# Optimization experiments

Hardware: AMD Instinct MI355X
Metric: run time of the kernel (lower is better)

## Reference

```python
import jax, jax.numpy as jnp
import numpy as np

N_NODES = 100000
N_EDGES = 600000
D_IN = 128
D_OUT = 128


def setup_inputs() -> dict:
    key = jax.random.key(0)
    ks = jax.random.split(key, 8)
    stdv = 1.0 / np.sqrt(D_OUT)
    return {
        "x": jax.random.normal(ks[0], (N_NODES, D_IN), dtype=jnp.float32),
        "edge_src": jax.random.randint(ks[1], (N_EDGES,), 0, N_NODES, dtype=jnp.int32),
        "edge_dst": jax.random.randint(ks[2], (N_EDGES,), 0, N_NODES, dtype=jnp.int32),
        "edge_weight": jax.random.uniform(ks[3], (N_EDGES,), dtype=jnp.float32),
        "weight_l": jax.random.uniform(ks[4], (D_IN, D_OUT), minval=-stdv, maxval=stdv, dtype=jnp.float32),
        "bias_l": jax.random.uniform(ks[5], (D_OUT,), minval=-stdv, maxval=stdv, dtype=jnp.float32),
        "weight_r": jax.random.uniform(ks[6], (D_IN, D_OUT), minval=-stdv, maxval=stdv, dtype=jnp.float32),
        "bias_r": jax.random.uniform(ks[7], (D_OUT,), minval=-stdv, maxval=stdv, dtype=jnp.float32),
    }


def reference(x, edge_src, edge_dst, edge_weight, weight_l, bias_l, weight_r, bias_r):
    # h = input @ weight_l  -> [N, D_OUT]
    h = x @ weight_l
    # spmm(adj, h): out[dst] += adj[dst, src] * h[src]
    msgs = h[edge_src] * edge_weight[:, None]          # [E, D_OUT] gather
    agg = jax.ops.segment_sum(msgs, edge_dst, num_segments=N_NODES)
    out = agg + bias_l
    # root_weight branch (size is None)
    out = out + x @ weight_r + bias_r
    return out
```

## Files before the change

kernel.cpp:

```cpp
#include <hip/hip_runtime.h>
#include <hip/hip_bf16.h>

#define D 128
#define SCAN_BLK 256
#define SCAN_VPT 4
#define SCAN_TILE (SCAN_BLK * SCAN_VPT)

typedef __attribute__((ext_vector_type(8))) short short8;
typedef __attribute__((ext_vector_type(4))) float f32x4;

__global__ __launch_bounds__(256) void prep_w(
    const float* __restrict__ Wl, const float* __restrict__ Wr,
    const float* __restrict__ bl, const float* __restrict__ br,
    __hip_bfloat16* __restrict__ WTl, __hip_bfloat16* __restrict__ WTr,
    float* __restrict__ bsum, int* __restrict__ deg, int n_nodes) {
  const int tid = blockIdx.x * 256 + threadIdx.x;
  const int n = (tid >> 7) & 127;
  const int k = tid & 127;
  if (tid < 16384) {
    WTl[n * D + k] = __float2bfloat16(Wl[k * D + n]);
  } else {
    WTr[n * D + k] = __float2bfloat16(Wr[k * D + n]);
  }
  if (tid < 128) bsum[tid] = bl[tid] + br[tid];
  for (int i = tid; i < n_nodes; i += 32768) deg[i] = 0;
}

__global__ __launch_bounds__(256) void gemm_hr(
    const float* __restrict__ x, const __hip_bfloat16* __restrict__ WTl,
    const __hip_bfloat16* __restrict__ WTr, const float* __restrict__ bsum,
    __hip_bfloat16* __restrict__ h, float* __restrict__ out,
    const int* __restrict__ edst, int* __restrict__ deg, int n_edges,
    int n_rowtiles) {
  const int gsz = gridDim.x * 256;
  for (int e = blockIdx.x * 256 + threadIdx.x; e < n_edges; e += gsz)
    atomicAdd(&deg[edst[e]], 1);

  __shared__ __hip_bfloat16 xs[16][136];
  const int t = threadIdx.x;
  const int wave = t >> 6;
  const int lane = t & 63;
  const int m = lane & 15;
  const int q = lane >> 4;

  short8 bfl[2][4], bfr[2][4];
  float bias[2];
#pragma unroll
  for (int c = 0; c < 2; ++c) {
    const int n0 = wave * 32 + c * 16;
    bias[c] = bsum[n0 + m];
#pragma unroll
    for (int ks = 0; ks < 4; ++ks) {
      bfl[c][ks] = *(const short8*)&WTl[(n0 + m) * D + ks * 32 + q * 8];
      bfr[c][ks] = *(const short8*)&WTr[(n0 + m) * D + ks * 32 + q * 8];
    }
  }

  const int srow = t >> 4;
  const int scol = (t & 15) * 8;

  for (int rt = blockIdx.x; rt < n_rowtiles; rt += gridDim.x) {
    const int rowbase = rt * 16;
    {
      const float4* src = (const float4*)&x[(size_t)(rowbase + srow) * D + scol];
      const float4 v0 = src[0], v1 = src[1];
      __hip_bfloat16* dst = &xs[srow][scol];
      dst[0] = __float2bfloat16(v0.x); dst[1] = __float2bfloat16(v0.y);
      dst[2] = __float2bfloat16(v0.z); dst[3] = __float2bfloat16(v0.w);
      dst[4] = __float2bfloat16(v1.x); dst[5] = __float2bfloat16(v1.y);
      dst[6] = __float2bfloat16(v1.z); dst[7] = __float2bfloat16(v1.w);
    }
    __syncthreads();

    f32x4 accL[2], accR[2];
#pragma unroll
    for (int c = 0; c < 2; ++c)
#pragma unroll
      for (int r = 0; r < 4; ++r) { accL[c][r] = 0.f; accR[c][r] = 0.f; }

#pragma unroll
    for (int ks = 0; ks < 4; ++ks) {
      const short8 afrag = *(const short8*)&xs[m][ks * 32 + q * 8];
#pragma unroll
      for (int c = 0; c < 2; ++c) {
        accL[c] = __builtin_amdgcn_mfma_f32_16x16x32_bf16(afrag, bfl[c][ks], accL[c], 0, 0, 0);
        accR[c] = __builtin_amdgcn_mfma_f32_16x16x32_bf16(afrag, bfr[c][ks], accR[c], 0, 0, 0);
      }
    }

#pragma unroll
    for (int c = 0; c < 2; ++c) {
      const int n = wave * 32 + c * 16 + m;
#pragma unroll
      for (int r = 0; r < 4; ++r) {
        const size_t row = (size_t)(rowbase + q * 4 + r);
        h[row * D + n] = __float2bfloat16(accL[c][r]);
        out[row * D + n] = accR[c][r] + bias[c];
      }
    }
    __syncthreads();
  }
}

__global__ __launch_bounds__(SCAN_BLK) void scan1_kernel(
    const int* __restrict__ deg, int* __restrict__ offsets,
    int* __restrict__ partials, int n) {
  __shared__ int sdata[SCAN_BLK];
  const int t = threadIdx.x;
  const int base = blockIdx.x * SCAN_TILE + t * SCAN_VPT;

  int v[SCAN_VPT];
  int s = 0;
#pragma unroll
  for (int j = 0; j < SCAN_VPT; ++j) {
    v[j] = (base + j < n) ? deg[base + j] : 0;
    s += v[j];
  }
  sdata[t] = s;
  __syncthreads();
  for (int off = 1; off < SCAN_BLK; off <<= 1) {
    int xv = (t >= off) ? sdata[t - off] : 0;
    __syncthreads();
    sdata[t] += xv;
    __syncthreads();
  }
  int excl = sdata[t] - s;
  if (t == SCAN_BLK - 1) partials[blockIdx.x] = sdata[t];
  int run = excl;
#pragma unroll
  for (int j = 0; j < SCAN_VPT; ++j) {
    if (base + j < n) offsets[base + j] = run;
    run += v[j];
  }
}

__global__ __launch_bounds__(SCAN_BLK) void scan3_kernel(
    int* __restrict__ offsets, int* __restrict__ pos,
    const int* __restrict__ partials, int n, int n_edges) {
  __shared__ int s_add;
  const int t = threadIdx.x;
  if (t < 64) {
    int v = 0;
    for (int j = t; j < blockIdx.x; j += 64) v += partials[j];
#pragma unroll
    for (int off = 32; off > 0; off >>= 1) v += __shfl_down(v, off);
    if (t == 0) s_add = v;
  }
  __syncthreads();
  const int add = s_add;
  const int base = blockIdx.x * SCAN_TILE + t * SCAN_VPT;
#pragma unroll
  for (int j = 0; j < SCAN_VPT; ++j) {
    const int i = base + j;
    if (i < n) {
      const int o = offsets[i] + add;
      offsets[i] = o;
      pos[i] = o;
    }
  }
  if (blockIdx.x == 0 && t == 0) offsets[n] = n_edges;
}

__global__ __launch_bounds__(256) void scatter_kernel(
    const int* __restrict__ esrc, const int* __restrict__ edst,
    const float* __restrict__ ew, int* __restrict__ pos,
    int2* __restrict__ pairs, int n_edges) {
  const int e = blockIdx.x * 256 + threadIdx.x;
  if (e >= n_edges) return;
  const int d = edst[e];
  const int slot = atomicAdd(&pos[d], 1);
  pairs[slot] = make_int2(esrc[e], __float_as_int(ew[e]));
}

__global__ __launch_bounds__(256) void sage_agg(
    const __hip_bfloat16* __restrict__ h,
    const int* __restrict__ offsets, const int2* __restrict__ pairs,
    float* __restrict__ out, int n_nodes) {
  const int node = blockIdx.x * 4 + (threadIdx.x >> 6);
  const int lane = threadIdx.x & 63;
  if (node >= n_nodes) return;
  const int begin = offsets[node];
  const int end = offsets[node + 1];
  const __hip_bfloat162* __restrict__ h2 = (const __hip_bfloat162*)h;

  float2 a = *(const float2*)&out[(size_t)node * D + 2 * lane];

  int i = begin;
  for (; i + 8 <= end; i += 8) {
    int2 p[8];
#pragma unroll
    for (int u = 0; u < 8; ++u) p[u] = pairs[i + u];
    __hip_bfloat162 hv[8];
#pragma unroll
    for (int u = 0; u < 8; ++u)
      hv[u] = h2[(size_t)p[u].x * (D / 2) + lane];
#pragma unroll
    for (int u = 0; u < 8; ++u) {
      const float w = __int_as_float(p[u].y);
      a.x = fmaf(w, __bfloat162float(hv[u].x), a.x);
      a.y = fmaf(w, __bfloat162float(hv[u].y), a.y);
    }
  }
  if (i < end) {
    int2 p[8];
#pragma unroll
    for (int u = 0; u < 8; ++u) {
      const int ei = (i + u < end) ? (i + u) : (end - 1);
      p[u] = pairs[ei];
      if (i + u >= end) p[u].y = 0;
    }
    __hip_bfloat162 hv[8];
#pragma unroll
    for (int u = 0; u < 8; ++u)
      hv[u] = h2[(size_t)p[u].x * (D / 2) + lane];
#pragma unroll
    for (int u = 0; u < 8; ++u) {
      const float w = __int_as_float(p[u].y);
      a.x = fmaf(w, __bfloat162float(hv[u].x), a.x);
      a.y = fmaf(w, __bfloat162float(hv[u].y), a.y);
    }
  }

  *(float2*)&out[(size_t)node * D + 2 * lane] = a;
}

extern "C" void kernel_launch(void* const* d_in, const int* in_sizes, int n_in,
                              void* d_out, int out_size, void* d_ws, size_t ws_size,
                              hipStream_t stream) {
  const float* x   = (const float*)d_in[0];
  const int* esrc  = (const int*)d_in[1];
  const int* edst  = (const int*)d_in[2];
  const float* ew  = (const float*)d_in[3];
  const float* Wl  = (const float*)d_in[4];
  const float* bl  = (const float*)d_in[5];
  const float* Wr  = (const float*)d_in[6];
  const float* br  = (const float*)d_in[7];
  float* out = (float*)d_out;

  const int n_nodes = in_sizes[0] / D;
  const int n_edges = in_sizes[1];

  char* ws = (char*)d_ws;
  size_t off = 0;
  __hip_bfloat16* h = (__hip_bfloat16*)(ws + off);
  off += (size_t)n_nodes * D * sizeof(__hip_bfloat16);
  off = (off + 15) & ~15ull;
  int* offsets = (int*)(ws + off);
  off += (size_t)(n_nodes + 1) * sizeof(int);
  off = (off + 15) & ~15ull;
  int* pos = (int*)(ws + off);
  off += (size_t)n_nodes * sizeof(int);
  off = (off + 15) & ~15ull;
  int* partials = (int*)(ws + off);
  off += 1024 * sizeof(int);
  off = (off + 15) & ~15ull;
  int2* pairs = (int2*)(ws + off);
  off += (size_t)n_edges * sizeof(int2);
  off = (off + 15) & ~15ull;
  __hip_bfloat16* WTl = (__hip_bfloat16*)(ws + off);
  off += (size_t)D * D * sizeof(__hip_bfloat16);
  __hip_bfloat16* WTr = (__hip_bfloat16*)(ws + off);
  off += (size_t)D * D * sizeof(__hip_bfloat16);
  float* bsum = (float*)(ws + off);
  off += D * sizeof(float);

  const int n_rowtiles = (n_nodes + 15) / 16;

  prep_w<<<128, 256, 0, stream>>>(Wl, Wr, bl, br, WTl, WTr, bsum, pos, n_nodes);

  const int gemm_grid = n_rowtiles < 2048 ? n_rowtiles : 2048;
  gemm_hr<<<gemm_grid, 256, 0, stream>>>(x, WTl, WTr, bsum, h, out, edst, pos,
                                         n_edges, n_rowtiles);

  const int nparts = (n_nodes + SCAN_TILE - 1) / SCAN_TILE;
  scan1_kernel<<<nparts, SCAN_BLK, 0, stream>>>(pos, offsets, partials, n_nodes);
  scan3_kernel<<<nparts, SCAN_BLK, 0, stream>>>(offsets, pos, partials, n_nodes, n_edges);
  scatter_kernel<<<(n_edges + 255) / 256, 256, 0, stream>>>(esrc, edst, ew, pos, pairs, n_edges);

  sage_agg<<<(n_nodes + 3) / 4, 256, 0, stream>>>(h, offsets, pairs, out, n_nodes);
}
```

Before: 236.7 us.

## Aggregate bf16 inputs first then fuse both projections into aggregation kernel

Reorders the computation so the neighbor aggregation runs on a bf16 copy of x, followed by a fused MFMA step that multiplies the aggregate by W_l and x by W_r in the same block. This removes the separate GEMM kernel's fp32 output write and the later read-modify-write of out. The aggregate is rounded to bf16 before the matmul, which adds rounding error. Each wave now processes two nodes sequentially, and the kernel assumes the node count is a multiple of 16.

Result: slower. 269.6 us (+13.9%).

```diff
diff --git a/kernel.cpp b/kernel.cpp
--- a/kernel.cpp
+++ b/kernel.cpp
@@ -8,6 +8,12 @@
 
 typedef __attribute__((ext_vector_type(8))) short short8;
 typedef __attribute__((ext_vector_type(4))) float f32x4;
+typedef __attribute__((ext_vector_type(4))) unsigned short ushort4v;
+
+static __device__ __forceinline__ unsigned short f2b(float f) {
+  __hip_bfloat16 b = __float2bfloat16(f);
+  return *reinterpret_cast<unsigned short*>(&b);
+}
 
 __global__ __launch_bounds__(256) void prep_w(
     const float* __restrict__ Wl, const float* __restrict__ Wr,
@@ -26,79 +32,22 @@
   for (int i = tid; i < n_nodes; i += 32768) deg[i] = 0;
 }
 
-__global__ __launch_bounds__(256) void gemm_hr(
-    const float* __restrict__ x, const __hip_bfloat16* __restrict__ WTl,
-    const __hip_bfloat16* __restrict__ WTr, const float* __restrict__ bsum,
-    __hip_bfloat16* __restrict__ h, float* __restrict__ out,
-    const int* __restrict__ edst, int* __restrict__ deg, int n_edges,
-    int n_rowtiles) {
+__global__ __launch_bounds__(256) void xb_hist(
+    const float* __restrict__ x, __hip_bfloat16* __restrict__ xb,
+    const int* __restrict__ edst, int* __restrict__ deg,
+    int n_nodes, int n_edges) {
   const int gsz = gridDim.x * 256;
-  for (int e = blockIdx.x * 256 + threadIdx.x; e < n_edges; e += gsz)
+  const int tid = blockIdx.x * 256 + threadIdx.x;
+  for (int e = tid; e < n_edges; e += gsz)
     atomicAdd(&deg[edst[e]], 1);
 
-  __shared__ __hip_bfloat16 xs[16][136];
-  const int t = threadIdx.x;
-  const int wave = t >> 6;
-  const int lane = t & 63;
-  const int m = lane & 15;
-  const int q = lane >> 4;
-
-  short8 bfl[2][4], bfr[2][4];
-  float bias[2];
-#pragma unroll
-  for (int c = 0; c < 2; ++c) {
-    const int n0 = wave * 32 + c * 16;
-    bias[c] = bsum[n0 + m];
-#pragma unroll
-    for (int ks = 0; ks < 4; ++ks) {
-      bfl[c][ks] = *(const short8*)&WTl[(n0 + m) * D + ks * 32 + q * 8];
-      bfr[c][ks] = *(const short8*)&WTr[(n0 + m) * D + ks * 32 + q * 8];
-    }
-  }
-
-  const int srow = t >> 4;
-  const int scol = (t & 15) * 8;
-
-  for (int rt = blockIdx.x; rt < n_rowtiles; rt += gridDim.x) {
-    const int rowbase = rt * 16;
-    {
-      const float4* src = (const float4*)&x[(size_t)(rowbase + srow) * D + scol];
-      const float4 v0 = src[0], v1 = src[1];
-      __hip_bfloat16* dst = &xs[srow][scol];
-      dst[0] = __float2bfloat16(v0.x); dst[1] = __float2bfloat16(v0.y);
-      dst[2] = __float2bfloat16(v0.z); dst[3] = __float2bfloat16(v0.w);
-      dst[4] = __float2bfloat16(v1.x); dst[5] = __float2bfloat16(v1.y);
-      dst[6] = __float2bfloat16(v1.z); dst[7] = __float2bfloat16(v1.w);
-    }
-    __syncthreads();
-
-    f32x4 accL[2], accR[2];
-#pragma unroll
-    for (int c = 0; c < 2; ++c)
-#pragma unroll
-      for (int r = 0; r < 4; ++r) { accL[c][r] = 0.f; accR[c][r] = 0.f; }
-
-#pragma unroll
-    for (int ks = 0; ks < 4; ++ks) {
-      const short8 afrag = *(const short8*)&xs[m][ks * 32 + q * 8];
-#pragma unroll
-      for (int c = 0; c < 2; ++c) {
-        accL[c] = __builtin_amdgcn_mfma_f32_16x16x32_bf16(afrag, bfl[c][ks], accL[c], 0, 0, 0);
-        accR[c] = __builtin_amdgcn_mfma_f32_16x16x32_bf16(afrag, bfr[c][ks], accR[c], 0, 0, 0);
-      }
-    }
-
-#pragma unroll
-    for (int c = 0; c < 2; ++c) {
-      const int n = wave * 32 + c * 16 + m;
-#pragma unroll
-      for (int r = 0; r < 4; ++r) {
-        const size_t row = (size_t)(rowbase + q * 4 + r);
-        h[row * D + n] = __float2bfloat16(accL[c][r]);
-        out[row * D + n] = accR[c][r] + bias[c];
-      }
-    }
-    __syncthreads();
+  const int total = n_nodes * (D / 4);
+  const float4* __restrict__ x4 = (const float4*)x;
+  for (int i = tid; i < total; i += gsz) {
+    const float4 v = x4[i];
+    ushort4v o;
+    o.x = f2b(v.x); o.y = f2b(v.y); o.z = f2b(v.z); o.w = f2b(v.w);
+    *reinterpret_cast<ushort4v*>(&xb[(size_t)i * 4]) = o;
   }
 }
 
@@ -172,56 +121,102 @@
   pairs[slot] = make_int2(esrc[e], __float_as_int(ew[e]));
 }
 
-__global__ __launch_bounds__(256) void sage_agg(
-    const __hip_bfloat16* __restrict__ h,
+__global__ __launch_bounds__(512) void sage_fused(
+    const __hip_bfloat16* __restrict__ xb,
+    const __hip_bfloat16* __restrict__ WTl,
+    const __hip_bfloat16* __restrict__ WTr,
+    const float* __restrict__ bsum,
     const int* __restrict__ offsets, const int2* __restrict__ pairs,
-    float* __restrict__ out, int n_nodes) {
-  const int node = blockIdx.x * 4 + (threadIdx.x >> 6);
-  const int lane = threadIdx.x & 63;
-  if (node >= n_nodes) return;
-  const int begin = offsets[node];
-  const int end = offsets[node + 1];
-  const __hip_bfloat162* __restrict__ h2 = (const __hip_bfloat162*)h;
-
-  float2 a = *(const float2*)&out[(size_t)node * D + 2 * lane];
-
-  int i = begin;
-  for (; i + 8 <= end; i += 8) {
-    int2 p[8];
-#pragma unroll
-    for (int u = 0; u < 8; ++u) p[u] = pairs[i + u];
-    __hip_bfloat162 hv[8];
-#pragma unroll
-    for (int u = 0; u < 8; ++u)
-      hv[u] = h2[(size_t)p[u].x * (D / 2) + lane];
-#pragma unroll
-    for (int u = 0; u < 8; ++u) {
-      const float w = __int_as_float(p[u].y);
-      a.x = fmaf(w, __bfloat162float(hv[u].x), a.x);
-      a.y = fmaf(w, __bfloat162float(hv[u].y), a.y);
+    float* __restrict__ out) {
+  __shared__ __hip_bfloat16 ga[16][136];
+  __shared__ __hip_bfloat16 xs[16][136];
+  const int t = threadIdx.x;
+  const int wave = t >> 6;
+  const int lane = t & 63;
+  const int m = lane & 15;
+  const int q = lane >> 4;
+  const int rowbase = blockIdx.x * 16;
+
+  const int n0 = wave * 16;
+  short8 bfl[4], bfr[4];
+#pragma unroll
+  for (int ks = 0; ks < 4; ++ks) {
+    bfl[ks] = *(const short8*)&WTl[(n0 + m) * D + ks * 32 + q * 8];
+    bfr[ks] = *(const short8*)&WTr[(n0 + m) * D + ks * 32 + q * 8];
+  }
+
+  if (t < 256) {
+    const int row = t >> 4;
+    const int c = (t & 15) * 8;
+    *(short8*)&xs[row][c] = *(const short8*)&xb[(size_t)(rowbase + row) * D + c];
+  }
+
+  const __hip_bfloat162* __restrict__ h2 = (const __hip_bfloat162*)xb;
+#pragma unroll
+  for (int j = 0; j < 2; ++j) {
+    const int ln = wave * 2 + j;
+    const int node = rowbase + ln;
+    const int begin = offsets[node];
+    const int end = offsets[node + 1];
+
+    float2 a = make_float2(0.f, 0.f);
+    int i = begin;
+    for (; i + 8 <= end; i += 8) {
+      int2 p[8];
+#pragma unroll
+      for (int u = 0; u < 8; ++u) p[u] = pairs[i + u];
+      __hip_bfloat162 hv[8];
+#pragma unroll
+      for (int u = 0; u < 8; ++u)
+        hv[u] = h2[(size_t)p[u].x * (D / 2) + lane];
+#pragma unroll
+      for (int u = 0; u < 8; ++u) {
+        const float w = __int_as_float(p[u].y);
+        a.x = fmaf(w, __bfloat162float(hv[u].x), a.x);
+        a.y = fmaf(w, __bfloat162float(hv[u].y), a.y);
+      }
     }
-  }
-  if (i < end) {
-    int2 p[8];
-#pragma unroll
-    for (int u = 0; u < 8; ++u) {
-      const int ei = (i + u < end) ? (i + u) : (end - 1);
-      p[u] = pairs[ei];
-      if (i + u >= end) p[u].y = 0;
+    if (i < end) {
+      int2 p[8];
+#pragma unroll
+      for (int u = 0; u < 8; ++u) {
+        const int ei = (i + u < end) ? (i + u) : (end - 1);
+        p[u] = pairs[ei];
+        if (i + u >= end) p[u].y = 0;
+      }
+      __hip_bfloat162 hv[8];
+#pragma unroll
+      for (int u = 0; u < 8; ++u)
+        hv[u] = h2[(size_t)p[u].x * (D / 2) + lane];
+#pragma unroll
+      for (int u = 0; u < 8; ++u) {
+        const float w = __int_as_float(p[u].y);
+        a.x = fmaf(w, __bfloat162float(hv[u].x), a.x);
+        a.y = fmaf(w, __bfloat162float(hv[u].y), a.y);
+      }
     }
-    __hip_bfloat162 hv[8];
-#pragma unroll
-    for (int u = 0; u < 8; ++u)
-      hv[u] = h2[(size_t)p[u].x * (D / 2) + lane];
-#pragma unroll
-    for (int u = 0; u < 8; ++u) {
-      const float w = __int_as_float(p[u].y);
-      a.x = fmaf(w, __bfloat162float(hv[u].x), a.x);
-      a.y = fmaf(w, __bfloat162float(hv[u].y), a.y);
-    }
-  }
-
-  *(float2*)&out[(size_t)node * D + 2 * lane] = a;
+    __hip_bfloat162 bv;
+    bv.x = __float2bfloat16(a.x);
+    bv.y = __float2bfloat16(a.y);
+    *(__hip_bfloat162*)&ga[ln][2 * lane] = bv;
+  }
+  __syncthreads();
+
+  f32x4 acc;
+#pragma unroll
+  for (int r = 0; r < 4; ++r) acc[r] = 0.f;
+#pragma unroll
+  for (int ks = 0; ks < 4; ++ks) {
+    const short8 aA = *(const short8*)&ga[m][ks * 32 + q * 8];
+    const short8 aX = *(const short8*)&xs[m][ks * 32 + q * 8];
+    acc = __builtin_amdgcn_mfma_f32_16x16x32_bf16(aA, bfl[ks], acc, 0, 0, 0);
+    acc = __builtin_amdgcn_mfma_f32_16x16x32_bf16(aX, bfr[ks], acc, 0, 0, 0);
+  }
+
+  const float bias = bsum[n0 + m];
+#pragma unroll
+  for (int r = 0; r < 4; ++r)
+    out[(size_t)(rowbase + q * 4 + r) * D + n0 + m] = acc[r] + bias;
 }
 
 extern "C" void kernel_launch(void* const* d_in, const int* in_sizes, int n_in,
@@ -242,7 +237,7 @@
 
   char* ws = (char*)d_ws;
   size_t off = 0;
-  __hip_bfloat16* h = (__hip_bfloat16*)(ws + off);
+  __hip_bfloat16* xb = (__hip_bfloat16*)(ws + off);
   off += (size_t)n_nodes * D * sizeof(__hip_bfloat16);
   off = (off + 15) & ~15ull;
   int* offsets = (int*)(ws + off);
@@ -268,14 +263,12 @@
 
   prep_w<<<128, 256, 0, stream>>>(Wl, Wr, bl, br, WTl, WTr, bsum, pos, n_nodes);
 
-  const int gemm_grid = n_rowtiles < 2048 ? n_rowtiles : 2048;
-  gemm_hr<<<gemm_grid, 256, 0, stream>>>(x, WTl, WTr, bsum, h, out, edst, pos,
-                                         n_edges, n_rowtiles);
+  xb_hist<<<2048, 256, 0, stream>>>(x, xb, edst, pos, n_nodes, n_edges);
 
   const int nparts = (n_nodes + SCAN_TILE - 1) / SCAN_TILE;
   scan1_kernel<<<nparts, SCAN_BLK, 0, stream>>>(pos, offsets, partials, n_nodes);
   scan3_kernel<<<nparts, SCAN_BLK, 0, stream>>>(offsets, pos, partials, n_nodes, n_edges);
   scatter_kernel<<<(n_edges + 255) / 256, 256, 0, stream>>>(esrc, edst, ew, pos, pairs, n_edges);
 
-  sage_agg<<<(n_nodes + 3) / 4, 256, 0, stream>>>(h, offsets, pairs, out, n_nodes);
-}
+  sage_fused<<<n_rowtiles, 512, 0, stream>>>(xb, WTl, WTr, bsum, offsets, pairs, out);
+}
```

## Fuse scan into single-pass decoupled look-back and retile GEMM to 32 rows per block

Applied to the files above, without the earlier changes.

Replaces the two-kernel block scan (partials then add) with one kernel that uses decoupled look-back over a per-block status array, removing a launch and a pass over offsets. The GEMM kernel now processes a single 32-row tile per block instead of grid-striding over 16-row tiles, and stages the bf16 h output through shared memory for coalesced 16-byte stores. The degree counting becomes one edge per thread. Risks are spin-waiting on block ordering and reloading weight fragments in every block.

After: 239.8 us. About the same (+1.3%).

```diff
diff --git a/kernel.cpp b/kernel.cpp
--- a/kernel.cpp
+++ b/kernel.cpp
@@ -13,7 +13,8 @@
     const float* __restrict__ Wl, const float* __restrict__ Wr,
     const float* __restrict__ bl, const float* __restrict__ br,
     __hip_bfloat16* __restrict__ WTl, __hip_bfloat16* __restrict__ WTr,
-    float* __restrict__ bsum, int* __restrict__ deg, int n_nodes) {
+    float* __restrict__ bsum, int* __restrict__ deg,
+    unsigned long long* __restrict__ state, int n_nodes) {
   const int tid = blockIdx.x * 256 + threadIdx.x;
   const int n = (tid >> 7) & 127;
   const int k = tid & 127;
@@ -23,6 +24,7 @@
     WTr[n * D + k] = __float2bfloat16(Wr[k * D + n]);
   }
   if (tid < 128) bsum[tid] = bl[tid] + br[tid];
+  if (tid < 1024) state[tid] = 0ull;
   for (int i = tid; i < n_nodes; i += 32768) deg[i] = 0;
 }
 
@@ -30,18 +32,17 @@
     const float* __restrict__ x, const __hip_bfloat16* __restrict__ WTl,
     const __hip_bfloat16* __restrict__ WTr, const float* __restrict__ bsum,
     __hip_bfloat16* __restrict__ h, float* __restrict__ out,
-    const int* __restrict__ edst, int* __restrict__ deg, int n_edges,
-    int n_rowtiles) {
-  const int gsz = gridDim.x * 256;
-  for (int e = blockIdx.x * 256 + threadIdx.x; e < n_edges; e += gsz)
-    atomicAdd(&deg[edst[e]], 1);
-
-  __shared__ __hip_bfloat16 xs[16][136];
+    const int* __restrict__ edst, int* __restrict__ deg, int n_edges) {
   const int t = threadIdx.x;
+  const int tid = blockIdx.x * 256 + t;
+  if (tid < n_edges) atomicAdd(&deg[edst[tid]], 1);
+
+  __shared__ __hip_bfloat16 xs[32][136];
   const int wave = t >> 6;
   const int lane = t & 63;
   const int m = lane & 15;
   const int q = lane >> 4;
+  const int rowbase = blockIdx.x * 32;
 
   short8 bfl[2][4], bfr[2][4];
   float bias[2];
@@ -56,64 +57,78 @@
     }
   }
 
-  const int srow = t >> 4;
-  const int scol = (t & 15) * 8;
-
-  for (int rt = blockIdx.x; rt < n_rowtiles; rt += gridDim.x) {
-    const int rowbase = rt * 16;
-    {
-      const float4* src = (const float4*)&x[(size_t)(rowbase + srow) * D + scol];
-      const float4 v0 = src[0], v1 = src[1];
-      __hip_bfloat16* dst = &xs[srow][scol];
-      dst[0] = __float2bfloat16(v0.x); dst[1] = __float2bfloat16(v0.y);
-      dst[2] = __float2bfloat16(v0.z); dst[3] = __float2bfloat16(v0.w);
-      dst[4] = __float2bfloat16(v1.x); dst[5] = __float2bfloat16(v1.y);
-      dst[6] = __float2bfloat16(v1.z); dst[7] = __float2bfloat16(v1.w);
-    }
-    __syncthreads();
-
-    f32x4 accL[2], accR[2];
+  const int srow = t >> 3;
+  const int scol = (t & 7) * 16;
+  {
+    const float4* src = (const float4*)&x[(size_t)(rowbase + srow) * D + scol];
+    const float4 v0 = src[0], v1 = src[1], v2 = src[2], v3 = src[3];
+    __hip_bfloat16* dst = &xs[srow][scol];
+    dst[0]  = __float2bfloat16(v0.x); dst[1]  = __float2bfloat16(v0.y);
+    dst[2]  = __float2bfloat16(v0.z); dst[3]  = __float2bfloat16(v0.w);
+    dst[4]  = __float2bfloat16(v1.x); dst[5]  = __float2bfloat16(v1.y);
+    dst[6]  = __float2bfloat16(v1.z); dst[7]  = __float2bfloat16(v1.w);
+    dst[8]  = __float2bfloat16(v2.x); dst[9]  = __float2bfloat16(v2.y);
+    dst[10] = __float2bfloat16(v2.z); dst[11] = __float2bfloat16(v2.w);
+    dst[12] = __float2bfloat16(v3.x); dst[13] = __float2bfloat16(v3.y);
+    dst[14] = __float2bfloat16(v3.z); dst[15] = __float2bfloat16(v3.w);
+  }
+  __syncthreads();
+
+  f32x4 aL[2][2], aR[2][2];
+#pragma unroll
+  for (int hf = 0; hf < 2; ++hf)
 #pragma unroll
     for (int c = 0; c < 2; ++c)
 #pragma unroll
-      for (int r = 0; r < 4; ++r) { accL[c][r] = 0.f; accR[c][r] = 0.f; }
-
+      for (int r = 0; r < 4; ++r) { aL[hf][c][r] = 0.f; aR[hf][c][r] = 0.f; }
+
+#pragma unroll
+  for (int hf = 0; hf < 2; ++hf) {
 #pragma unroll
     for (int ks = 0; ks < 4; ++ks) {
-      const short8 afrag = *(const short8*)&xs[m][ks * 32 + q * 8];
+      const short8 afrag = *(const short8*)&xs[hf * 16 + m][ks * 32 + q * 8];
 #pragma unroll
       for (int c = 0; c < 2; ++c) {
-        accL[c] = __builtin_amdgcn_mfma_f32_16x16x32_bf16(afrag, bfl[c][ks], accL[c], 0, 0, 0);
-        accR[c] = __builtin_amdgcn_mfma_f32_16x16x32_bf16(afrag, bfr[c][ks], accR[c], 0, 0, 0);
+        aL[hf][c] = __builtin_amdgcn_mfma_f32_16x16x32_bf16(afrag, bfl[c][ks], aL[hf][c], 0, 0, 0);
+        aR[hf][c] = __builtin_amdgcn_mfma_f32_16x16x32_bf16(afrag, bfr[c][ks], aR[hf][c], 0, 0, 0);
       }
     }
-
+  }
+  __syncthreads();
+
+#pragma unroll
+  for (int hf = 0; hf < 2; ++hf) {
 #pragma unroll
     for (int c = 0; c < 2; ++c) {
       const int n = wave * 32 + c * 16 + m;
 #pragma unroll
       for (int r = 0; r < 4; ++r) {
-        const size_t row = (size_t)(rowbase + q * 4 + r);
-        h[row * D + n] = __float2bfloat16(accL[c][r]);
-        out[row * D + n] = accR[c][r] + bias[c];
+        const int row = hf * 16 + q * 4 + r;
+        out[(size_t)(rowbase + row) * D + n] = aR[hf][c][r] + bias[c];
+        xs[row][n] = __float2bfloat16(aL[hf][c][r]);
       }
     }
-    __syncthreads();
-  }
-}
-
-__global__ __launch_bounds__(SCAN_BLK) void scan1_kernel(
-    const int* __restrict__ deg, int* __restrict__ offsets,
-    int* __restrict__ partials, int n) {
+  }
+  __syncthreads();
+
+  *(short8*)&h[(size_t)(rowbase + srow) * D + scol] = *(const short8*)&xs[srow][scol];
+  *(short8*)&h[(size_t)(rowbase + srow) * D + scol + 8] = *(const short8*)&xs[srow][scol + 8];
+}
+
+__global__ __launch_bounds__(SCAN_BLK) void scan_ll(
+    int* __restrict__ pos , int* __restrict__ offsets,
+    unsigned long long* __restrict__ state, int n, int n_edges) {
   __shared__ int sdata[SCAN_BLK];
+  __shared__ int s_prefix;
   const int t = threadIdx.x;
-  const int base = blockIdx.x * SCAN_TILE + t * SCAN_VPT;
+  const int b = blockIdx.x;
+  const int base = b * SCAN_TILE + t * SCAN_VPT;
 
   int v[SCAN_VPT];
   int s = 0;
 #pragma unroll
   for (int j = 0; j < SCAN_VPT; ++j) {
-    v[j] = (base + j < n) ? deg[base + j] : 0;
+    v[j] = (base + j < n) ? pos[base + j] : 0;
     s += v[j];
   }
   sdata[t] = s;
@@ -124,41 +139,66 @@
     sdata[t] += xv;
     __syncthreads();
   }
-  int excl = sdata[t] - s;
-  if (t == SCAN_BLK - 1) partials[blockIdx.x] = sdata[t];
-  int run = excl;
+  const int excl = sdata[t] - s;
+  const int total = sdata[SCAN_BLK - 1];
+
+  if (t == 0) {
+    const unsigned long long st =
+        ((unsigned long long)(b == 0 ? 2 : 1) << 62) | (unsigned int)total;
+    __hip_atomic_store(&state[b], st, __ATOMIC_RELEASE, __HIP_MEMORY_SCOPE_AGENT);
+  }
+
+  if (b == 0) {
+    if (t == 0) s_prefix = 0;
+  } else if (t < 64) {
+    int windowEnd = b;
+    int acc = 0;
+    for (;;) {
+      const int j = windowEnd - 1 - t;
+      unsigned long long st = 0;
+      if (j >= 0) {
+        do {
+          st = __hip_atomic_load(&state[j], __ATOMIC_ACQUIRE, __HIP_MEMORY_SCOPE_AGENT);
+        } while (st == 0);
+      }
+      const int flag = (j >= 0) ? (int)(st >> 62) : 2;
+      const int val = (j >= 0) ? (int)(st & 0xffffffffull) : 0;
+      const unsigned long long mask = __ballot(flag == 2);
+      if (mask) {
+        const int firstLane = __ffsll((long long)mask) - 1;
+        int contrib = (t <= firstLane) ? val : 0;
+#pragma unroll
+        for (int o = 32; o > 0; o >>= 1) contrib += __shfl_down(contrib, o);
+        if (t == 0) { acc += contrib; s_prefix = acc; }
+        break;
+      } else {
+        int contrib = val;
+#pragma unroll
+        for (int o = 32; o > 0; o >>= 1) contrib += __shfl_down(contrib, o);
+        if (t == 0) acc += contrib;
+        windowEnd -= 64;
+      }
+    }
+  }
+  __syncthreads();
+  const int add = s_prefix;
+
+  if (t == 0 && b > 0) {
+    const unsigned long long st =
+        (2ull << 62) | (unsigned int)(add + total);
+    __hip_atomic_store(&state[b], st, __ATOMIC_RELEASE, __HIP_MEMORY_SCOPE_AGENT);
+  }
+
+  int run = add + excl;
 #pragma unroll
   for (int j = 0; j < SCAN_VPT; ++j) {
-    if (base + j < n) offsets[base + j] = run;
+    if (base + j < n) {
+      offsets[base + j] = run;
+      pos[base + j] = run;
+    }
     run += v[j];
   }
-}
-
-__global__ __launch_bounds__(SCAN_BLK) void scan3_kernel(
-    int* __restrict__ offsets, int* __restrict__ pos,
-    const int* __restrict__ partials, int n, int n_edges) {
-  __shared__ int s_add;
-  const int t = threadIdx.x;
-  if (t < 64) {
-    int v = 0;
-    for (int j = t; j < blockIdx.x; j += 64) v += partials[j];
-#pragma unroll
-    for (int off = 32; off > 0; off >>= 1) v += __shfl_down(v, off);
-    if (t == 0) s_add = v;
-  }
-  __syncthreads();
-  const int add = s_add;
-  const int base = blockIdx.x * SCAN_TILE + t * SCAN_VPT;
-#pragma unroll
-  for (int j = 0; j < SCAN_VPT; ++j) {
-    const int i = base + j;
-    if (i < n) {
-      const int o = offsets[i] + add;
-      offsets[i] = o;
-      pos[i] = o;
-    }
-  }
-  if (blockIdx.x == 0 && t == 0) offsets[n] = n_edges;
+  if (b == 0 && t == 0) offsets[n] = n_edges;
 }
 
 __global__ __launch_bounds__(256) void scatter_kernel(
@@ -251,8 +291,8 @@
   int* pos = (int*)(ws + off);
   off += (size_t)n_nodes * sizeof(int);
   off = (off + 15) & ~15ull;
-  int* partials = (int*)(ws + off);
-  off += 1024 * sizeof(int);
+  unsigned long long* state = (unsigned long long*)(ws + off);
+  off += 1024 * sizeof(unsigned long long);
   off = (off + 15) & ~15ull;
   int2* pairs = (int2*)(ws + off);
   off += (size_t)n_edges * sizeof(int2);
@@ -264,17 +304,14 @@
   float* bsum = (float*)(ws + off);
   off += D * sizeof(float);
 
-  const int n_rowtiles = (n_nodes + 15) / 16;
-
-  prep_w<<<128, 256, 0, stream>>>(Wl, Wr, bl, br, WTl, WTr, bsum, pos, n_nodes);
-
-  const int gemm_grid = n_rowtiles < 2048 ? n_rowtiles : 2048;
-  gemm_hr<<<gemm_grid, 256, 0, stream>>>(x, WTl, WTr, bsum, h, out, edst, pos,
-                                         n_edges, n_rowtiles);
+  prep_w<<<128, 256, 0, stream>>>(Wl, Wr, bl, br, WTl, WTr, bsum, pos, state, n_nodes);
+
+  const int n_tiles32 = (n_nodes + 31) / 32;
+  gemm_hr<<<n_tiles32, 256, 0, stream>>>(x, WTl, WTr, bsum, h, out, edst, pos, n_edges);
 
   const int nparts = (n_nodes + SCAN_TILE - 1) / SCAN_TILE;
-  scan1_kernel<<<nparts, SCAN_BLK, 0, stream>>>(pos, offsets, partials, n_nodes);
-  scan3_kernel<<<nparts, SCAN_BLK, 0, stream>>>(offsets, pos, partials, n_nodes, n_edges);
+  scan_ll<<<nparts, SCAN_BLK, 0, stream>>>(pos, offsets, state, n_nodes, n_edges);
+
   scatter_kernel<<<(n_edges + 255) / 256, 256, 0, stream>>>(esrc, edst, ew, pos, pairs, n_edges);
 
   sage_agg<<<(n_nodes + 3) / 4, 256, 0, stream>>>(h, offsets, pairs, out, n_nodes);
```
